# Optimization experiments

Measured on AMD Instinct MI355X. Metric: run time of the kernel, lower is better.

The kernel has to match this reference:

```python
import jax, jax.numpy as jnp
import numpy as np

N, F, K = 256, 32, 8
B = 65536


def setup_inputs() -> dict:
    key = jax.random.key(0)
    k1, k2, k3, k4 = jax.random.split(key, 4)
    x = jax.random.normal(k1, (B, N), dtype=jnp.float32)
    w_lin = jax.random.normal(k2, (N,), dtype=jnp.float32)
    b_lin = jax.random.normal(k3, (1,), dtype=jnp.float32)
    v = jax.random.normal(k4, (N, F, K), dtype=jnp.float32)
    # feature -> field mapping, matching feature2fielddict = {i: i % F}
    field_idx = jnp.arange(N, dtype=jnp.int32) % F
    return {"x": x, "w_lin": w_lin, "b_lin": b_lin, "v": v, "field_idx": field_idx}


def reference(x, w_lin, b_lin, v, field_idx):
    # linear part: nn.Linear(n, 1)
    linear_part = x @ w_lin[:, None] + b_lin  # [B, 1]
    # A[i, j] = v[i, field[j]]  -> [n, n, k]
    A = v[:, field_idx, :]
    # Wmat[i, j] = <v[i, field[j]], v[j, field[i]]>
    Wmat = jnp.einsum('ijk,jik->ij', A, A)  # [n, n]
    # only strict upper triangle (i < j) contributes
    Wu = jnp.triu(Wmat, k=1)
    # sum_{i<j} Wmat[i,j] * x[:,i] * x[:,j]
    interaction = jnp.einsum('bi,ij,bj->b', x, Wu, x)[:, None]  # [B, 1]
    return linear_part + interaction
```

## Files before the change

### kernel.cpp

```cpp
#include <hip/hip_runtime.h>
#include <hip/hip_bf16.h>


#define FK 256

typedef __attribute__((ext_vector_type(8))) short bf16x8;
typedef __attribute__((ext_vector_type(4))) float f32x4v;

__device__ __forceinline__ unsigned short f2bf(float x) {
    return __builtin_bit_cast(unsigned short, __float2bfloat16(x));
}
__device__ __forceinline__ float bf2f(unsigned short h) {
    return __builtin_bit_cast(float, (unsigned int)h << 16);
}

template<int CTRL>
__device__ __forceinline__ float dppadd(float v) {
    int t = __builtin_amdgcn_update_dpp(0, __builtin_bit_cast(int, v),
                                        CTRL, 0xf, 0xf, true);
    return v + __builtin_bit_cast(float, t);
}

__device__ __forceinline__ void block_sync_novm() {
    asm volatile("s_waitcnt lgkmcnt(0)\n\ts_barrier" ::: "memory");
}

__global__ __launch_bounds__(128) void k_build_m(
    const float* __restrict__ v, const int* __restrict__ fidx,
    unsigned int* __restrict__ mp)
{
    __shared__ int fsh[256];
    int tid = threadIdx.x;
    fsh[tid] = fidx[tid];
    fsh[tid + 128] = fidx[tid + 128];
    __syncthreads();

    int u = blockIdx.x * 128 + tid;
    int f  = u >> 2;
    int l  = f & 63;
    int ct = (f >> 6) & 15;
    int s  = f >> 10;
    int c  = ct * 16 + (l & 15);
    int i80 = (u & 3) * 2;
    int k0 = s * 32 + ((l >> 4) & 3) * 8 + i80;
    int fc = fsh[c];
    unsigned short hh[2];
#pragma unroll
    for (int i = 0; i < 2; ++i) {
        int k = k0 + i;
        float acc = 0.f;
        if (k != c) {
            int fk = fsh[k];
            const float* va = v + k * FK + fc * 8;
            const float* vb = v + c * FK + fk * 8;
#pragma unroll
            for (int j = 0; j < 8; ++j) acc += va[j] * vb[j];
            acc *= 0.5f;
        }
        hh[i] = f2bf(acc);
    }
    mp[u] = (unsigned int)hh[0] | ((unsigned int)hh[1] << 16);
}


__device__ __forceinline__ void stage_tile(unsigned short* buf,
                                           const float4* pre,
                                           int row, int l15) {
    char* b = (char*)buf;
#pragma unroll
    for (int j = 0; j < 4; ++j) {
        unsigned long long h0 = f2bf(pre[j].x), h1 = f2bf(pre[j].y),
                           h2 = f2bf(pre[j].z), h3 = f2bf(pre[j].w);
        unsigned long long pk = h0 | (h1 << 16) | (h2 << 32) | (h3 << 48);
        int chunkB = (l15 >> 1) + 8 * j;
        int off = row * 512 + ((chunkB ^ (row & 7)) << 4) + (l15 & 1) * 8;
        *(unsigned long long*)(b + off) = pk;
    }
}

__global__ __launch_bounds__(256, 2) void k_main(
    const float* __restrict__ x, const float* __restrict__ w_lin,
    const float* __restrict__ b_lin, const uint4* __restrict__ mpack,
    float* __restrict__ out)
{
    __shared__ unsigned short xs[2][4096];
    __shared__ float part[2][4][16];

    const int tid = threadIdx.x;
    const int w   = tid >> 6;
    const int l   = tid & 63;
    const int l15 = l & 15;
    const int lg  = l >> 4;

    const long rowbase = (long)blockIdx.x * 128;
    const float* xg = x + rowbase * 256;

    const int srow = w * 4 + lg;

    float4 pre[4];
#pragma unroll
    for (int j = 0; j < 4; ++j)
        pre[j] = *(const float4*)(xg + srow * 256 + (l15 + 16 * j) * 4);

    bf16x8 Brg[8][4];
#pragma unroll
    for (int s = 0; s < 8; ++s)
#pragma unroll
        for (int c = 0; c < 4; ++c)
            Brg[s][c] = __builtin_bit_cast(bf16x8,
                mpack[(s * 16 + w * 4 + c) * 64 + l]);

    float wv4[4];
#pragma unroll
    for (int c = 0; c < 4; ++c)
        wv4[c] = w_lin[(w * 4 + c) * 16 + l15];
    const float bv = b_lin[0];

    stage_tile(xs[0], pre, srow, l15);
#pragma unroll
    for (int j = 0; j < 4; ++j)
        pre[j] = *(const float4*)(xg + (16 + srow) * 256 + (l15 + 16 * j) * 4);
    block_sync_novm();

    for (int t = 0; t < 8; ++t) {
        const char* xsb = (const char*)xs[t & 1];

        f32x4v acc[4];
#pragma unroll
        for (int c = 0; c < 4; ++c)
            acc[c] = f32x4v{wv4[c], wv4[c], wv4[c], wv4[c]};
#pragma unroll
        for (int s = 0; s < 8; ++s) {
            int aoff = l15 * 512 + ((s * 64 + lg * 16) ^ ((l15 & 7) << 4));
            bf16x8 af = *(const bf16x8*)(xsb + aoff);
            acc[0] = __builtin_amdgcn_mfma_f32_16x16x32_bf16(af, Brg[s][0], acc[0], 0, 0, 0);
            acc[1] = __builtin_amdgcn_mfma_f32_16x16x32_bf16(af, Brg[s][1], acc[1], 0, 0, 0);
            acc[2] = __builtin_amdgcn_mfma_f32_16x16x32_bf16(af, Brg[s][2], acc[2], 0, 0, 0);
            acc[3] = __builtin_amdgcn_mfma_f32_16x16x32_bf16(af, Brg[s][3], acc[3], 0, 0, 0);
        }

#pragma unroll
        for (int r = 0; r < 4; ++r) {
            int row = lg * 4 + r;
            int sw  = (row & 7) << 4;
            float pp = 0.f;
#pragma unroll
            for (int c = 0; c < 4; ++c) {
                int col = (w * 4 + c) * 16 + l15;
                unsigned short h = *(const unsigned short*)(xsb + row * 512 + ((col * 2) ^ sw));
                pp += bf2f(h) * acc[c][r];
            }
            pp = dppadd<0x121>(pp); pp = dppadd<0x122>(pp);
            pp = dppadd<0x124>(pp); pp = dppadd<0x128>(pp);
            if (l15 == 0) part[t & 1][w][row] = pp;
        }

        if (t < 7)
            stage_tile(xs[(t + 1) & 1], pre, srow, l15);
        if (t < 6) {
#pragma unroll
            for (int j = 0; j < 4; ++j)
                pre[j] = *(const float4*)(xg + ((t + 2) * 16 + srow) * 256 + (l15 + 16 * j) * 4);
        }
        block_sync_novm();

        if (tid < 16) {
            float y = part[t & 1][0][tid] + part[t & 1][1][tid] +
                      part[t & 1][2][tid] + part[t & 1][3][tid];
            out[rowbase + t * 16 + tid] = y + bv;
        }
    }
}

extern "C" void kernel_launch(void* const* d_in, const int* in_sizes, int n_in,
                              void* d_out, int out_size, void* d_ws, size_t ws_size,
                              hipStream_t stream) {
    const float* x     = (const float*)d_in[0];
    const float* w_lin = (const float*)d_in[1];
    const float* b_lin = (const float*)d_in[2];
    const float* v     = (const float*)d_in[3];
    const int*   fidx  = (const int*)d_in[4];
    float* out = (float*)d_out;
    void* mpack = d_ws;

    k_build_m<<<256, 128, 0, stream>>>(v, fidx, (unsigned int*)mpack);
    k_main<<<512, 256, 0, stream>>>(x, w_lin, b_lin, (const uint4*)mpack, out);
}
```

Baseline: 23.73 us.

## Process 32-row tiles per iteration and simplify M-build to one element per thread

The main kernel now stages and computes two 16-row sub-tiles (32 rows) per loop iteration, halving the iteration count and barriers while reusing the register-resident B fragments across both sub-tiles. Shared memory for the x tile and partial sums doubles, and the prefetch register buffer doubles. The M-build kernel is restructured so each of 256 threads computes one bf16 element instead of two packed ones. The cost is higher register and LDS pressure, which may reduce occupancy under the 2-blocks-per-CU launch bound.

```diff
diff --git a/kernel.cpp b/kernel.cpp
--- a/kernel.cpp
+++ b/kernel.cpp
@@ -25,56 +25,54 @@
     asm volatile("s_waitcnt lgkmcnt(0)\n\ts_barrier" ::: "memory");
 }
 
-__global__ __launch_bounds__(128) void k_build_m(
+__global__ __launch_bounds__(256) void k_build_m(
     const float* __restrict__ v, const int* __restrict__ fidx,
-    unsigned int* __restrict__ mp)
+    unsigned short* __restrict__ mp)
 {
     __shared__ int fsh[256];
     int tid = threadIdx.x;
     fsh[tid] = fidx[tid];
-    fsh[tid + 128] = fidx[tid + 128];
     __syncthreads();
 
-    int u = blockIdx.x * 128 + tid;
-    int f  = u >> 2;
-    int l  = f & 63;
-    int ct = (f >> 6) & 15;
-    int s  = f >> 10;
+    int e  = blockIdx.x * 256 + tid;
+    int i8 = e & 7;
+    int l  = (e >> 3) & 63;
+    int ct = (e >> 9) & 15;
+    int s  = e >> 13;
     int c  = ct * 16 + (l & 15);
-    int i80 = (u & 3) * 2;
-    int k0 = s * 32 + ((l >> 4) & 3) * 8 + i80;
-    int fc = fsh[c];
-    unsigned short hh[2];
-#pragma unroll
-    for (int i = 0; i < 2; ++i) {
-        int k = k0 + i;
-        float acc = 0.f;
-        if (k != c) {
-            int fk = fsh[k];
-            const float* va = v + k * FK + fc * 8;
-            const float* vb = v + c * FK + fk * 8;
-#pragma unroll
-            for (int j = 0; j < 8; ++j) acc += va[j] * vb[j];
-            acc *= 0.5f;
-        }
-        hh[i] = f2bf(acc);
+    int k  = s * 32 + ((l >> 4) & 3) * 8 + i8;
+
+    float acc = 0.f;
+    if (k != c) {
+        int fc = fsh[c];
+        int fk = fsh[k];
+        const float* va = v + k * FK + fc * 8;
+        const float* vb = v + c * FK + fk * 8;
+#pragma unroll
+        for (int j = 0; j < 8; ++j) acc += va[j] * vb[j];
+        acc *= 0.5f;
     }
-    mp[u] = (unsigned int)hh[0] | ((unsigned int)hh[1] << 16);
-}
-
-
-__device__ __forceinline__ void stage_tile(unsigned short* buf,
-                                           const float4* pre,
-                                           int row, int l15) {
+    mp[e] = f2bf(acc);
+}
+
+
+__device__ __forceinline__ void stage_tile32(unsigned short* buf,
+                                             const float4* pre,
+                                             int srow, int l15) {
     char* b = (char*)buf;
 #pragma unroll
-    for (int j = 0; j < 4; ++j) {
-        unsigned long long h0 = f2bf(pre[j].x), h1 = f2bf(pre[j].y),
-                           h2 = f2bf(pre[j].z), h3 = f2bf(pre[j].w);
-        unsigned long long pk = h0 | (h1 << 16) | (h2 << 32) | (h3 << 48);
-        int chunkB = (l15 >> 1) + 8 * j;
-        int off = row * 512 + ((chunkB ^ (row & 7)) << 4) + (l15 & 1) * 8;
-        *(unsigned long long*)(b + off) = pk;
+    for (int h = 0; h < 2; ++h) {
+        int row = srow + h * 16;
+#pragma unroll
+        for (int j = 0; j < 4; ++j) {
+            const float4 val = pre[h * 4 + j];
+            unsigned long long h0 = f2bf(val.x), h1 = f2bf(val.y),
+                               h2 = f2bf(val.z), h3 = f2bf(val.w);
+            unsigned long long pk = h0 | (h1 << 16) | (h2 << 32) | (h3 << 48);
+            int chunkB = (l15 >> 1) + 8 * j;
+            int off = row * 512 + ((chunkB ^ (row & 7)) << 4) + (l15 & 1) * 8;
+            *(unsigned long long*)(b + off) = pk;
+        }
     }
 }
 
@@ -83,8 +81,8 @@
     const float* __restrict__ b_lin, const uint4* __restrict__ mpack,
     float* __restrict__ out)
 {
-    __shared__ unsigned short xs[2][4096];
-    __shared__ float part[2][4][16];
+    __shared__ unsigned short xs[2][8192];
+    __shared__ float part[2][4][32];
 
     const int tid = threadIdx.x;
     const int w   = tid >> 6;
@@ -97,10 +95,12 @@
 
     const int srow = w * 4 + lg;
 
-    float4 pre[4];
-#pragma unroll
-    for (int j = 0; j < 4; ++j)
-        pre[j] = *(const float4*)(xg + srow * 256 + (l15 + 16 * j) * 4);
+    float4 pre[8];
+#pragma unroll
+    for (int h = 0; h < 2; ++h)
+#pragma unroll
+        for (int j = 0; j < 4; ++j)
+            pre[h * 4 + j] = *(const float4*)(xg + (srow + h * 16) * 256 + (l15 + 16 * j) * 4);
 
     bf16x8 Brg[8][4];
 #pragma unroll
@@ -116,58 +116,70 @@
         wv4[c] = w_lin[(w * 4 + c) * 16 + l15];
     const float bv = b_lin[0];
 
-    stage_tile(xs[0], pre, srow, l15);
-#pragma unroll
-    for (int j = 0; j < 4; ++j)
-        pre[j] = *(const float4*)(xg + (16 + srow) * 256 + (l15 + 16 * j) * 4);
+    stage_tile32(xs[0], pre, srow, l15);
+#pragma unroll
+    for (int h = 0; h < 2; ++h)
+#pragma unroll
+        for (int j = 0; j < 4; ++j)
+            pre[h * 4 + j] = *(const float4*)(xg + (32 + srow + h * 16) * 256 + (l15 + 16 * j) * 4);
     block_sync_novm();
 
-    for (int t = 0; t < 8; ++t) {
+    for (int t = 0; t < 4; ++t) {
         const char* xsb = (const char*)xs[t & 1];
 
-        f32x4v acc[4];
-#pragma unroll
-        for (int c = 0; c < 4; ++c)
-            acc[c] = f32x4v{wv4[c], wv4[c], wv4[c], wv4[c]};
+        f32x4v acc[2][4];
+#pragma unroll
+        for (int rt = 0; rt < 2; ++rt)
+#pragma unroll
+            for (int c = 0; c < 4; ++c)
+                acc[rt][c] = f32x4v{wv4[c], wv4[c], wv4[c], wv4[c]};
 #pragma unroll
         for (int s = 0; s < 8; ++s) {
-            int aoff = l15 * 512 + ((s * 64 + lg * 16) ^ ((l15 & 7) << 4));
-            bf16x8 af = *(const bf16x8*)(xsb + aoff);
-            acc[0] = __builtin_amdgcn_mfma_f32_16x16x32_bf16(af, Brg[s][0], acc[0], 0, 0, 0);
-            acc[1] = __builtin_amdgcn_mfma_f32_16x16x32_bf16(af, Brg[s][1], acc[1], 0, 0, 0);
-            acc[2] = __builtin_amdgcn_mfma_f32_16x16x32_bf16(af, Brg[s][2], acc[2], 0, 0, 0);
-            acc[3] = __builtin_amdgcn_mfma_f32_16x16x32_bf16(af, Brg[s][3], acc[3], 0, 0, 0);
-        }
-
-#pragma unroll
-        for (int r = 0; r < 4; ++r) {
-            int row = lg * 4 + r;
-            int sw  = (row & 7) << 4;
-            float pp = 0.f;
-#pragma unroll
-            for (int c = 0; c < 4; ++c) {
-                int col = (w * 4 + c) * 16 + l15;
-                unsigned short h = *(const unsigned short*)(xsb + row * 512 + ((col * 2) ^ sw));
-                pp += bf2f(h) * acc[c][r];
+            int koff = (s * 64 + lg * 16) ^ ((l15 & 7) << 4);
+#pragma unroll
+            for (int rt = 0; rt < 2; ++rt) {
+                bf16x8 af = *(const bf16x8*)(xsb + (rt * 16 + l15) * 512 + koff);
+                acc[rt][0] = __builtin_amdgcn_mfma_f32_16x16x32_bf16(af, Brg[s][0], acc[rt][0], 0, 0, 0);
+                acc[rt][1] = __builtin_amdgcn_mfma_f32_16x16x32_bf16(af, Brg[s][1], acc[rt][1], 0, 0, 0);
+                acc[rt][2] = __builtin_amdgcn_mfma_f32_16x16x32_bf16(af, Brg[s][2], acc[rt][2], 0, 0, 0);
+                acc[rt][3] = __builtin_amdgcn_mfma_f32_16x16x32_bf16(af, Brg[s][3], acc[rt][3], 0, 0, 0);
             }
-            pp = dppadd<0x121>(pp); pp = dppadd<0x122>(pp);
-            pp = dppadd<0x124>(pp); pp = dppadd<0x128>(pp);
-            if (l15 == 0) part[t & 1][w][row] = pp;
-        }
-
-        if (t < 7)
-            stage_tile(xs[(t + 1) & 1], pre, srow, l15);
-        if (t < 6) {
-#pragma unroll
-            for (int j = 0; j < 4; ++j)
-                pre[j] = *(const float4*)(xg + ((t + 2) * 16 + srow) * 256 + (l15 + 16 * j) * 4);
+        }
+
+#pragma unroll
+        for (int rt = 0; rt < 2; ++rt) {
+#pragma unroll
+            for (int r = 0; r < 4; ++r) {
+                int row = rt * 16 + lg * 4 + r;
+                int sw  = (row & 7) << 4;
+                float pp = 0.f;
+#pragma unroll
+                for (int c = 0; c < 4; ++c) {
+                    int col = (w * 4 + c) * 16 + l15;
+                    unsigned short h = *(const unsigned short*)(xsb + row * 512 + ((col * 2) ^ sw));
+                    pp += bf2f(h) * acc[rt][c][r];
+                }
+                pp = dppadd<0x121>(pp); pp = dppadd<0x122>(pp);
+                pp = dppadd<0x124>(pp); pp = dppadd<0x128>(pp);
+                if (l15 == 0) part[t & 1][w][row] = pp;
+            }
+        }
+
+        if (t < 3)
+            stage_tile32(xs[(t + 1) & 1], pre, srow, l15);
+        if (t < 2) {
+#pragma unroll
+            for (int h = 0; h < 2; ++h)
+#pragma unroll
+                for (int j = 0; j < 4; ++j)
+                    pre[h * 4 + j] = *(const float4*)(xg + ((t + 2) * 32 + srow + h * 16) * 256 + (l15 + 16 * j) * 4);
         }
         block_sync_novm();
 
-        if (tid < 16) {
+        if (tid < 32) {
             float y = part[t & 1][0][tid] + part[t & 1][1][tid] +
                       part[t & 1][2][tid] + part[t & 1][3][tid];
-            out[rowbase + t * 16 + tid] = y + bv;
+            out[rowbase + t * 32 + tid] = y + bv;
         }
     }
 }
@@ -183,6 +195,6 @@
     float* out = (float*)d_out;
     void* mpack = d_ws;
 
-    k_build_m<<<256, 128, 0, stream>>>(v, fidx, (unsigned int*)mpack);
+    k_build_m<<<256, 256, 0, stream>>>(v, fidx, (unsigned short*)mpack);
     k_main<<<512, 256, 0, stream>>>(x, w_lin, b_lin, (const uint4*)mpack, out);
 }
```

Result: slower. 44.86 us (+89.1%).
